# Optimization experiments

Hardware: AMD Instinct MI355X
Metric: run time of the kernel (lower is better)

## Reference

```python
import jax, jax.numpy as jnp
import numpy as np

NUM_CLASSES = 8
SCORE_T = 0.5
IOU_T = 0.5
POSE_HYPS = 10
MAX_DET = 100
B, A = 1, 4096


def _pairwise_iou(bx):
    # bx: (N,4) in (x1,y1,x2,y2); TF-style +1 pixel convention
    x1 = jnp.maximum(bx[:, None, 0], bx[None, :, 0])
    y1 = jnp.maximum(bx[:, None, 1], bx[None, :, 1])
    x2 = jnp.minimum(bx[:, None, 2], bx[None, :, 2])
    y2 = jnp.minimum(bx[:, None, 3], bx[None, :, 3])
    wid = x2 - x1 + 1.0
    hei = y2 - y1 + 1.0
    inter = wid * hei
    area = (bx[:, 2] - bx[:, 0] + 1.0) * (bx[:, 3] - bx[:, 1] + 1.0)
    den = area[:, None] + area[None, :] - inter
    ov = jnp.where(den == 0.0, 0.0, inter / jnp.where(den == 0.0, 1.0, den))  # divide_no_nan
    return jnp.where((wid <= 0.0) | (hei <= 0.0), 0.0, ov)


def _per_class(scores_c, boxes_c, poses_c, conf_c):
    # Fixed-shape re-expression of _filter_detections: instead of compacting the
    # boxes with score > threshold (dynamic shape), keep all N and mask invalid
    # boxes out of the overlap indicator. Relative ordering (which drives the
    # argmax tie-break and the ascending sort) is identical to the compacted
    # subset, so the math matches exactly.
    N = scores_c.shape[0]
    K = POSE_HYPS + 1
    valid = scores_c > SCORE_T
    m = jnp.sum(valid.astype(jnp.int32))  # number of selected boxes
    ov = _pairwise_iou(boxes_c)  # (N,N)
    ind = ((ov > IOU_T) & valid[:, None] & valid[None, :]).astype(jnp.float32)
    # scatter_nd: true_ov[argmax_col(row i), i] = max(row i); column i is unique per update
    max_col = jnp.argmax(ind, axis=1)
    true_ov = jnp.zeros_like(ind).at[max_col, jnp.arange(N)].add(jnp.max(ind, axis=1))
    bc = (1.0 - ov) * true_ov * conf_c[None, :]
    bc = jnp.where(bc == 0.0, 1000.0, bc)  # 1000 = sentinel for 'not a hypothesis'
    # Only the first min(pose_hyps+1, m) ascending-sorted entries per row survive the
    # sequence mask, so take the K smallest instead of a full argsort (same result;
    # top_k of the negation breaks ties by lowest index like a stable ascending sort).
    neg, args = jax.lax.top_k(-bc, K)
    svals = -neg  # (N,K) K smallest per row
    hyp = (jnp.arange(K) < jnp.minimum(K, m)).astype(jnp.float32)
    cmask = jnp.where(svals == 1000.0, 0.0, 1.0) * hyp[None, :]
    denom = jnp.sum(cmask, axis=1)  # (N,)
    safe = jnp.where(denom == 0.0, 1.0, denom)
    poses_avg = jnp.where(denom[:, None] == 0.0, 0.0,
                          jnp.sum(cmask[:, :, None] * poses_c[args], axis=1) / safe[:, None])
    boxes_avg = jnp.where(denom[:, None] == 0.0, 0.0,
                          jnp.sum(cmask[:, :, None] * boxes_c[args], axis=1) / safe[:, None])
    return poses_avg, boxes_avg, denom > 0.0


def _forward(boxes3D, boxes, classification, poses, confidence):
    C = NUM_CLASSES
    N = classification.shape[0] * classification.shape[1]
    cls = classification.reshape(N, C)
    bxs = boxes.reshape(N, C, 4)
    pss = poses.reshape(N, C, 12)
    cnf = confidence.reshape(N, C)
    # boxes3D is reshaped/gathered by the original but never used afterwards (dead code)
    xs = (cls.T, jnp.transpose(bxs, (1, 0, 2)), jnp.transpose(pss, (1, 0, 2)), cnf.T)
    # serialize over classes so only one NxN working set is live at a time
    poses_avg, boxes_avg, survive = jax.lax.map(lambda t: _per_class(*t), xs)
    surv = survive.reshape(-1)  # (C*N,) class-major, matching the original concat order
    count = jnp.sum(surv.astype(jnp.int32))
    scores_flat = jnp.where(surv, cls.T.reshape(-1), -jnp.inf)
    top_scores, _ = jax.lax.top_k(scores_flat, MAX_DET)
    rank = jnp.arange(MAX_DET)
    ok = rank < count
    out_scores = jnp.where(ok, top_scores, -1.0)
    # NOTE: the original computes top_indices but never applies it — labels/poses/
    # indices/boxes stay in class-major survivor order, truncated/padded with -1.
    pos = jnp.arange(C * N)
    order = jnp.argsort(jnp.where(surv, pos, pos + C * N))  # stable compaction
    sel = order[:MAX_DET]
    labels_flat = jnp.repeat(jnp.arange(C), N)
    anchors_flat = jnp.tile(jnp.arange(N), C)
    out_labels = jnp.where(ok, labels_flat[sel], -1).astype(jnp.int32)
    out_idx = jnp.where(ok, anchors_flat[sel], -1).astype(jnp.int32)
    out_poses = jnp.where(ok[:, None], poses_avg.reshape(C * N, 12)[sel], -1.0)
    out_boxes = jnp.where(ok[:, None], boxes_avg.reshape(C * N, 4)[sel], -1.0)
    return out_scores, out_labels, out_poses, out_idx, out_boxes


def setup_inputs():
    key = jax.random.key(0)
    k1, k2, k3, k4, k5, k6 = jax.random.split(key, 6)
    C = NUM_CLASSES
    # realistic heavily-overlapping boxes in a 640x640 image
    cxy = jax.random.uniform(k1, (B, A, C, 2), minval=0.0, maxval=640.0)
    wh = jax.random.uniform(k2, (B, A, C, 2), minval=10.0, maxval=120.0)
    boxes = jnp.concatenate([cxy - wh / 2.0, cxy + wh / 2.0], axis=-1).reshape(B, A, C * 4)
    return {
        "boxes3D": jax.random.normal(k6, (B, A, C * 16), dtype=jnp.float32),
        "boxes": boxes,
        "classification": jax.random.uniform(k3, (B, A, C), dtype=jnp.float32),
        "poses": jax.random.normal(k4, (B, A, C * 12), dtype=jnp.float32),
        "confidence": jax.random.uniform(k5, (B, A, C), dtype=jnp.float32),
    }


def reference(boxes3D, boxes, classification, poses, confidence):
    return _forward(boxes3D, boxes, classification, poses, confidence)
```

## Files before the change

### kernel.cpp

```cpp
#include <hip/hip_runtime.h>
#include <stdint.h>

#define N_ANCH 4096
#define NCLS 8
#define CN (N_ANCH * NCLS)
#define SCORE_TH 0.5f
#define IOU_TH 0.5f
#define KSEL 11
#define MAX_DET 100
#define CAND_CAP 4096
#define TI 128
#define TJ 64
#define JOBS_PER_CLASS 1056

struct Params {
    const float* boxes; const float* cls; const float* poses; const float* conf;
    int* validList; int* mVal; int* minRank;
    int* surv; int* hist; int* blockCnt; int* gcnt;
    int* rep; int* sel; int* count_g; float* cand;
    float* out;
};

__device__ __forceinline__ float area_f(float4 b) {
    return (b.z - b.x + 1.0f) * (b.w - b.y + 1.0f);
}

__device__ __forceinline__ float iou_f(float4 a, float areaA, float4 b, float areaB) {
    float x1 = fmaxf(a.x, b.x);
    float y1 = fmaxf(a.y, b.y);
    float x2 = fminf(a.z, b.z);
    float y2 = fminf(a.w, b.w);
    float wid = x2 - x1 + 1.0f;
    float hei = y2 - y1 + 1.0f;
    float inter = wid * hei;
    float den = areaA + areaB - inter;
    float ov = (den == 0.0f) ? 0.0f : (inter / den);
    if (wid <= 0.0f || hei <= 0.0f) ov = 0.0f;
    return ov;
}

__global__ void __launch_bounds__(256) kS(Params p) {
    const int c = blockIdx.x;
    const int tid = threadIdx.x;
    const int lane = tid & 63, w = tid >> 6;
    const int cbase = c << 12;
    __shared__ unsigned long long smask[64];
    __shared__ int sbase[16];

    for (int ch = 0; ch < 16; ch++) {
        int n = ch * 256 + tid;
        int flag = (p.cls[n * 8 + c] > SCORE_TH) ? 1 : 0;
        unsigned long long m = __ballot(flag);
        if (lane == 0) smask[ch * 4 + w] = m;
    }
    __syncthreads();
    if (tid == 0) {
        int run = 0;
        for (int ch = 0; ch < 16; ch++) {
            sbase[ch] = run;
            run += __popcll(smask[ch * 4]) + __popcll(smask[ch * 4 + 1]) +
                   __popcll(smask[ch * 4 + 2]) + __popcll(smask[ch * 4 + 3]);
        }
        p.mVal[c] = run;
    }
    __syncthreads();
    for (int ch = 0; ch < 16; ch++) {
        unsigned long long m = smask[ch * 4 + w];
        if ((m >> lane) & 1ull) {
            int rank = __popcll(m & ((1ull << lane) - 1ull));
            int wb = 0;
            for (int i = 0; i < w; i++) wb += __popcll(smask[ch * 4 + i]);
            p.validList[c * N_ANCH + sbase[ch] + wb + rank] = ch * 256 + tid;
        }
    }
    for (int i = tid; i < N_ANCH; i += 256) {
        p.surv[cbase + i] = 0;
        p.minRank[cbase + i] = 0x7FFFFFFF;
    }
    if (c == 0) {
        for (int i = tid; i < 1024; i += 256) p.hist[i] = 0;
        if (tid < 128) p.blockCnt[tid] = 0;
        if (tid == 0) *p.gcnt = 0;
    }
}

__global__ void __launch_bounds__(128) kM(Params p) {
    int bid = blockIdx.x;
    int c = bid / JOBS_PER_CLASS;
    int t = bid - c * JOBS_PER_CLASS;
    int ci = (int)((sqrtf(4.0f * (float)t + 1.0f) - 1.0f) * 0.5f);
    while ((ci + 1) * (ci + 2) <= t) ci++;
    while (ci * (ci + 1) > t) ci--;
    int jt = t - ci * (ci + 1);
    int mc = p.mVal[c];
    int ib = ci * TI, jb = jt * TJ;
    if (ib >= mc || jb >= mc) return;
    int tid = threadIdx.x;
    int cbase = c << 12;
    const int* vl = p.validList + cbase;
    const float4* boxes4 = (const float4*)p.boxes;
    __shared__ float4 sB[TJ];
    __shared__ float sA[TJ];
    if (tid < TJ && jb + tid < mc) {
        int vj = vl[jb + tid];
        float4 b = boxes4[vj * 8 + c];
        sB[tid] = b;
        sA[tid] = area_f(b);
    }
    __syncthreads();
    int i = ib + tid;
    if (i >= mc) return;
    int limit = min(TJ, i - jb);
    limit = min(limit, mc - jb);
    if (limit <= 0) return;
    int k = vl[i];
    float4 bk = boxes4[k * 8 + c];
    float ak = area_f(bk);
    int lmin = 0x7FFFFFFF;
    #pragma unroll 4
    for (int r = 0; r < limit; r++) {
        float4 bj = sB[r];
        float x1 = fmaxf(bk.x, bj.x);
        float y1 = fmaxf(bk.y, bj.y);
        float x2 = fminf(bk.z, bj.z);
        float y2 = fminf(bk.w, bj.w);
        float wid = x2 - x1 + 1.0f;
        float hei = y2 - y1 + 1.0f;
        float inter = wid * hei;
        float den = ak + sA[r] - inter;
        bool m = (wid > 0.0f) && (hei > 0.0f) && (inter > 0.5f * den);
        if (m && r < lmin) lmin = r;
    }
    if (lmin != 0x7FFFFFFF) atomicMin(&p.minRank[cbase + i], jb + lmin);
}

__global__ void __launch_bounds__(256) kF(Params p) {
    int t = blockIdx.x * 256 + threadIdx.x;
    int c = t >> 12;
    int i = t & (N_ANCH - 1);
    if (i >= p.mVal[c]) return;
    int cbase = c << 12;
    const int* vl = p.validList + cbase;
    const float4* boxes4 = (const float4*)p.boxes;
    int k = vl[i];
    int mr = p.minRank[t];
    if (mr > i) mr = i;
    int ja = vl[mr];
    p.rep[cbase + k] = ja;
    if (mr < i) {
        float4 bk = boxes4[k * 8 + c];
        float4 bj = boxes4[ja * 8 + c];
        float ov = iou_f(bk, area_f(bk), bj, area_f(bj));
        float bcv = (1.0f - ov) * p.conf[k * 8 + c];
        if (bcv != 0.0f) {
            int old = atomicExch(&p.surv[cbase + ja], 1);
            if (old == 0) {
                atomicAdd(&p.blockCnt[(cbase + ja) >> 8], 1);
                unsigned bits = __float_as_uint(p.cls[ja * 8 + c]);
                int bb = (int)((bits - 0x3F000000u) >> 13);
                int bkt = bb < 0 ? 0 : (bb > 1023 ? 1023 : bb);
                atomicAdd(&p.hist[bkt], 1);
            }
        }
    }
}

__global__ void __launch_bounds__(256) kG(Params p) {
    const int bid = blockIdx.x;
    const int tid = threadIdx.x;
    const int lane = tid & 63, w = tid >> 6;
    __shared__ int sCnt[128];
    __shared__ int sSfx[256];
    __shared__ int s_misc[8];

    if (tid == 0) s_misc[0] = 0;
    if (tid < 128) sCnt[tid] = p.blockCnt[tid];
    int part = p.hist[4 * tid] + p.hist[4 * tid + 1] +
               p.hist[4 * tid + 2] + p.hist[4 * tid + 3];
    sSfx[tid] = part;
    __syncthreads();
    if (tid == 0) {
        int run = 0, myoff = 0;
        for (int i = 0; i < 128; i++) {
            if (i == bid) myoff = run;
            run += sCnt[i];
        }
        s_misc[1] = run;
        s_misc[2] = myoff;
        if (bid == 0) *p.count_g = run;
        int run2 = 0;
        for (int i = 255; i >= 0; i--) { int v = sSfx[i]; sSfx[i] = run2; run2 += v; }
    }
    __syncthreads();
    int count = s_misc[1];
    int target = count < MAX_DET ? count : MAX_DET;
    int S = sSfx[tid];
    int found = -1;
    for (int b = 4 * tid + 3; b >= 4 * tid; b--) {
        S += p.hist[b];
        if (found < 0 && S >= target) found = b;
    }
    if (found >= 0) atomicMax(&s_misc[0], found);
    __syncthreads();
    int t0 = s_misc[0];

    int q = bid * 256 + tid;
    int c = q >> 12, n = q & (N_ANCH - 1);
    int flag = p.surv[q] != 0;
    unsigned long long mask = __ballot(flag);
    if (lane == 0) s_misc[4 + w] = __popcll(mask);
    __syncthreads();
    int rank = __popcll(mask & ((1ull << lane) - 1ull));
    int wbase = 0;
    for (int i = 0; i < w; i++) wbase += s_misc[4 + i];
    int idx = s_misc[2] + wbase + rank;
    if (flag && idx < MAX_DET) p.sel[idx] = q;
    if (flag) {
        float sc = p.cls[n * 8 + c];
        unsigned bits = __float_as_uint(sc);
        int bb = (int)((bits - 0x3F000000u) >> 13);
        int bkt = bb < 0 ? 0 : (bb > 1023 ? 1023 : bb);
        if (bkt >= t0) {
            int id = atomicAdd(p.gcnt, 1);
            if (id < CAND_CAP) p.cand[id] = sc;
        }
    }
}

__global__ void __launch_bounds__(256) kO(Params p) {
    const int bid = blockIdx.x;
    const int tid = threadIdx.x;
    const int lane = tid & 63, w = tid >> 6;
    __shared__ __align__(16) unsigned char SMEM[32768];
    __shared__ int s_misc[8];
    __shared__ int s_ksel[KSEL];
    __shared__ unsigned long long s_red[5];
    const float4* boxes4 = (const float4*)p.boxes;

    if (bid == 0) {
        float* s = (float*)SMEM;
        int cc = *p.gcnt; if (cc > CAND_CAP) cc = CAND_CAP;
        int count = *p.count_g;
        int n = 128; while (n < cc) n <<= 1;
        for (int i = tid; i < n; i += 256) s[i] = (i < cc) ? -p.cand[i] : 1e38f;
        __syncthreads();
        for (int kk = 2; kk <= n; kk <<= 1) {
            for (int jj = kk >> 1; jj > 0; jj >>= 1) {
                for (int i = tid; i < n; i += 256) {
                    int ixj = i ^ jj;
                    if (ixj > i) {
                        float a = s[i], b2 = s[ixj];
                        bool up = ((i & kk) == 0);
                        if (up ? (a > b2) : (a < b2)) { s[i] = b2; s[ixj] = a; }
                    }
                }
                __syncthreads();
            }
        }
        if (tid < MAX_DET) p.out[tid] = (tid < count) ? -s[tid] : -1.0f;
    } else {
        int s = bid - 1;
        int count = *p.count_g;
        if (s >= count) {
            if (tid == 0) { p.out[100 + s] = -1.0f; p.out[1400 + s] = -1.0f; }
            if (tid < 12) p.out[200 + s * 12 + tid] = -1.0f;
            if (tid >= 16 && tid < 20) p.out[1500 + s * 4 + (tid - 16)] = -1.0f;
        } else {
            int sp = p.sel[s];
            int c = sp >> 12;
            int r = sp & (N_ANCH - 1);
            int cbase = c << 12;
            unsigned long long* keyArr = (unsigned long long*)SMEM;
            if (tid == 0) s_misc[0] = 0;
            __syncthreads();
            float4 br = boxes4[r * 8 + c];
            float ar = area_f(br);
            for (int k = tid; k < N_ANCH; k += 256) {
                if (k != r && p.cls[k * 8 + c] > SCORE_TH && p.rep[cbase + k] == r) {
                    float4 bkk = boxes4[k * 8 + c];
                    float ov = iou_f(br, ar, bkk, area_f(bkk));
                    float bcv = (1.0f - ov) * p.conf[k * 8 + c];
                    if (bcv != 0.0f) {
                        int id = atomicAdd(&s_misc[0], 1);
                        keyArr[id] = ((unsigned long long)__float_as_uint(bcv) << 32) | (unsigned)k;
                    }
                }
            }
            __syncthreads();
            int nm = s_misc[0];
            int dn = nm < KSEL ? nm : KSEL;
            unsigned long long lastBest = ~0ull;
            for (int j = 0; j < dn; j++) {
                unsigned long long bk = ~0ull;
                for (int i = tid; i < nm; i += 256) {
                    unsigned long long v = keyArr[i];
                    if (v == lastBest) { keyArr[i] = ~0ull; v = ~0ull; }
                    if (v < bk) bk = v;
                }
                for (int off = 32; off > 0; off >>= 1) {
                    unsigned long long o = __shfl_down(bk, off);
                    if (o < bk) bk = o;
                }
                if (lane == 0) s_red[w] = bk;
                __syncthreads();
                if (tid == 0) {
                    unsigned long long B = s_red[0];
                    for (int q2 = 1; q2 < 4; q2++) if (s_red[q2] < B) B = s_red[q2];
                    s_red[4] = B;
                    s_ksel[j] = (int)(B & 0xFFFFFFFFull);
                }
                __syncthreads();
                lastBest = s_red[4];
            }
            float fdn = (float)(dn > 0 ? dn : 1);
            if (tid < 12) {
                float ssum = 0.0f;
                for (int j = 0; j < dn; j++) {
                    int k = s_ksel[j];
                    ssum += p.poses[(k * 8 + c) * 12 + tid];
                }
                p.out[200 + s * 12 + tid] = ssum / fdn;
            } else if (tid < 16) {
                int d = tid - 12;
                float ssum = 0.0f;
                for (int j = 0; j < dn; j++) {
                    int k = s_ksel[j];
                    const float* bb2 = (const float*)&boxes4[k * 8 + c];
                    ssum += bb2[d];
                }
                p.out[1500 + s * 4 + d] = ssum / fdn;
            } else if (tid == 16) {
                p.out[100 + s] = (float)c;
            } else if (tid == 17) {
                p.out[1400 + s] = (float)r;
            }
        }
    }
}

extern "C" void kernel_launch(void* const* d_in, const int* in_sizes, int n_in,
                              void* d_out, int out_size, void* d_ws, size_t ws_size,
                              hipStream_t stream) {
    Params hp;
    hp.boxes = (const float*)d_in[1];
    hp.cls   = (const float*)d_in[2];
    hp.poses = (const float*)d_in[3];
    hp.conf  = (const float*)d_in[4];
    hp.out   = (float*)d_out;

    char* ws = (char*)d_ws;
    size_t off = 0;
    auto alloc = [&](size_t bytes) {
        void* pp = ws + off;
        off += (bytes + 255) & ~(size_t)255;
        return pp;
    };
    hp.validList = (int*)alloc(CN * sizeof(int));
    hp.mVal      = (int*)alloc(64);
    hp.minRank   = (int*)alloc(CN * sizeof(int));
    hp.surv      = (int*)alloc(CN * sizeof(int));
    hp.hist      = (int*)alloc(1024 * sizeof(int));
    hp.blockCnt  = (int*)alloc(128 * sizeof(int));
    hp.gcnt      = (int*)alloc(64);
    hp.rep       = (int*)alloc(CN * sizeof(int));
    hp.sel       = (int*)alloc(MAX_DET * sizeof(int));
    hp.count_g   = (int*)alloc(64);
    hp.cand      = (float*)alloc(CAND_CAP * sizeof(float));

    kS<<<NCLS, 256, 0, stream>>>(hp);
    kM<<<NCLS * JOBS_PER_CLASS, TI, 0, stream>>>(hp);
    kF<<<CN / 256, 256, 0, stream>>>(hp);
    kG<<<CN / 256, 256, 0, stream>>>(hp);
    kO<<<MAX_DET + 1, 256, 0, stream>>>(hp);
}
```

Baseline: 121.5 us.

## Fuse compaction/threshold kernel into output kernel, removing one launch

Removes the kG kernel and folds its work into kO. Every kO block recomputes the prefix sum of per-chunk survivor counts and then locates its own selected detection through a ballot over a single 256-entry chunk. Block 0 now does the histogram threshold and gathers candidates into shared memory by scanning all 32K survivor flags serially before the bitonic sort. This saves a kernel launch and its global scratch traffic, but block 0 takes on a 128-iteration scan that may lengthen the critical path.

```diff
diff --git a/kernel.cpp b/kernel.cpp
--- a/kernel.cpp
+++ b/kernel.cpp
@@ -16,8 +16,8 @@
 struct Params {
     const float* boxes; const float* cls; const float* poses; const float* conf;
     int* validList; int* mVal; int* minRank;
-    int* surv; int* hist; int* blockCnt; int* gcnt;
-    int* rep; int* sel; int* count_g; float* cand;
+    int* surv; int* hist; int* blockCnt;
+    int* rep;
     float* out;
 };
 
@@ -80,7 +80,6 @@
     if (c == 0) {
         for (int i = tid; i < 1024; i += 256) p.hist[i] = 0;
         if (tid < 128) p.blockCnt[tid] = 0;
-        if (tid == 0) *p.gcnt = 0;
     }
 }
 
@@ -165,84 +164,71 @@
     }
 }
 
-__global__ void __launch_bounds__(256) kG(Params p) {
-    const int bid = blockIdx.x;
-    const int tid = threadIdx.x;
-    const int lane = tid & 63, w = tid >> 6;
-    __shared__ int sCnt[128];
-    __shared__ int sSfx[256];
-    __shared__ int s_misc[8];
-
-    if (tid == 0) s_misc[0] = 0;
-    if (tid < 128) sCnt[tid] = p.blockCnt[tid];
-    int part = p.hist[4 * tid] + p.hist[4 * tid + 1] +
-               p.hist[4 * tid + 2] + p.hist[4 * tid + 3];
-    sSfx[tid] = part;
-    __syncthreads();
-    if (tid == 0) {
-        int run = 0, myoff = 0;
-        for (int i = 0; i < 128; i++) {
-            if (i == bid) myoff = run;
-            run += sCnt[i];
-        }
-        s_misc[1] = run;
-        s_misc[2] = myoff;
-        if (bid == 0) *p.count_g = run;
-        int run2 = 0;
-        for (int i = 255; i >= 0; i--) { int v = sSfx[i]; sSfx[i] = run2; run2 += v; }
-    }
-    __syncthreads();
-    int count = s_misc[1];
-    int target = count < MAX_DET ? count : MAX_DET;
-    int S = sSfx[tid];
-    int found = -1;
-    for (int b = 4 * tid + 3; b >= 4 * tid; b--) {
-        S += p.hist[b];
-        if (found < 0 && S >= target) found = b;
-    }
-    if (found >= 0) atomicMax(&s_misc[0], found);
-    __syncthreads();
-    int t0 = s_misc[0];
-
-    int q = bid * 256 + tid;
-    int c = q >> 12, n = q & (N_ANCH - 1);
-    int flag = p.surv[q] != 0;
-    unsigned long long mask = __ballot(flag);
-    if (lane == 0) s_misc[4 + w] = __popcll(mask);
-    __syncthreads();
-    int rank = __popcll(mask & ((1ull << lane) - 1ull));
-    int wbase = 0;
-    for (int i = 0; i < w; i++) wbase += s_misc[4 + i];
-    int idx = s_misc[2] + wbase + rank;
-    if (flag && idx < MAX_DET) p.sel[idx] = q;
-    if (flag) {
-        float sc = p.cls[n * 8 + c];
-        unsigned bits = __float_as_uint(sc);
-        int bb = (int)((bits - 0x3F000000u) >> 13);
-        int bkt = bb < 0 ? 0 : (bb > 1023 ? 1023 : bb);
-        if (bkt >= t0) {
-            int id = atomicAdd(p.gcnt, 1);
-            if (id < CAND_CAP) p.cand[id] = sc;
-        }
-    }
-}
-
 __global__ void __launch_bounds__(256) kO(Params p) {
     const int bid = blockIdx.x;
     const int tid = threadIdx.x;
     const int lane = tid & 63, w = tid >> 6;
     __shared__ __align__(16) unsigned char SMEM[32768];
+    __shared__ int sCnt[128];
+    __shared__ int sSfx[256];
     __shared__ int s_misc[8];
+    __shared__ int s_sp;
     __shared__ int s_ksel[KSEL];
     __shared__ unsigned long long s_red[5];
     const float4* boxes4 = (const float4*)p.boxes;
 
+    if (tid < 128) sCnt[tid] = p.blockCnt[tid];
+    __syncthreads();
+    if (tid == 0) {
+        int run = 0;
+        for (int i = 0; i < 128; i++) { int v = sCnt[i]; sCnt[i] = run; run += v; }
+        s_misc[1] = run;
+    }
+    __syncthreads();
+    int count = s_misc[1];
+
     if (bid == 0) {
+        if (tid == 0) s_misc[0] = 0;
+        int part = p.hist[4 * tid] + p.hist[4 * tid + 1] +
+                   p.hist[4 * tid + 2] + p.hist[4 * tid + 3];
+        sSfx[tid] = part;
+        __syncthreads();
+        if (tid == 0) {
+            int run2 = 0;
+            for (int i = 255; i >= 0; i--) { int v = sSfx[i]; sSfx[i] = run2; run2 += v; }
+        }
+        __syncthreads();
+        int target = count < MAX_DET ? count : MAX_DET;
+        int S = sSfx[tid];
+        int found = -1;
+        for (int b = 4 * tid + 3; b >= 4 * tid; b--) {
+            S += p.hist[b];
+            if (found < 0 && S >= target) found = b;
+        }
+        if (found >= 0) atomicMax(&s_misc[0], found);
+        __syncthreads();
+        int t0 = s_misc[0];
         float* s = (float*)SMEM;
-        int cc = *p.gcnt; if (cc > CAND_CAP) cc = CAND_CAP;
-        int count = *p.count_g;
+        if (tid == 0) s_misc[2] = 0;
+        __syncthreads();
+        for (int base = 0; base < CN; base += 256) {
+            int q = base + tid;
+            if (p.surv[q] != 0) {
+                int c = q >> 12, n = q & (N_ANCH - 1);
+                float sc = p.cls[n * 8 + c];
+                unsigned bits = __float_as_uint(sc);
+                int bb = (int)((bits - 0x3F000000u) >> 13);
+                int bkt = bb < 0 ? 0 : (bb > 1023 ? 1023 : bb);
+                if (bkt >= t0) {
+                    int id = atomicAdd(&s_misc[2], 1);
+                    if (id < CAND_CAP) s[id] = sc;
+                }
+            }
+        }
+        __syncthreads();
+        int cc = s_misc[2]; if (cc > CAND_CAP) cc = CAND_CAP;
         int n = 128; while (n < cc) n <<= 1;
-        for (int i = tid; i < n; i += 256) s[i] = (i < cc) ? -p.cand[i] : 1e38f;
+        for (int i = tid; i < n; i += 256) s[i] = (i < cc) ? -s[i] : 1e38f;
         __syncthreads();
         for (int kk = 2; kk <= n; kk <<= 1) {
             for (int jj = kk >> 1; jj > 0; jj >>= 1) {
@@ -259,14 +245,31 @@
         }
         if (tid < MAX_DET) p.out[tid] = (tid < count) ? -s[tid] : -1.0f;
     } else {
-        int s = bid - 1;
-        int count = *p.count_g;
-        if (s >= count) {
-            if (tid == 0) { p.out[100 + s] = -1.0f; p.out[1400 + s] = -1.0f; }
-            if (tid < 12) p.out[200 + s * 12 + tid] = -1.0f;
-            if (tid >= 16 && tid < 20) p.out[1500 + s * 4 + (tid - 16)] = -1.0f;
+        int sIdx = bid - 1;
+        if (sIdx >= count) {
+            if (tid == 0) { p.out[100 + sIdx] = -1.0f; p.out[1400 + sIdx] = -1.0f; }
+            if (tid < 12) p.out[200 + sIdx * 12 + tid] = -1.0f;
+            if (tid >= 16 && tid < 20) p.out[1500 + sIdx * 4 + (tid - 16)] = -1.0f;
         } else {
-            int sp = p.sel[s];
+            if (tid == 0) {
+                int ch = 0;
+                for (int i = 0; i < 128; i++) { if (sCnt[i] <= sIdx) ch = i; else break; }
+                s_misc[3] = ch;
+            }
+            __syncthreads();
+            int ch = s_misc[3];
+            int ls = sIdx - sCnt[ch];
+            int qq = ch * 256 + tid;
+            int flag = p.surv[qq] != 0;
+            unsigned long long m = __ballot(flag);
+            if (lane == 0) s_misc[4 + w] = __popcll(m);
+            __syncthreads();
+            int wbase = 0;
+            for (int i = 0; i < w; i++) wbase += s_misc[4 + i];
+            int rank = wbase + __popcll(m & ((1ull << lane) - 1ull));
+            if (flag && rank == ls) s_sp = qq;
+            __syncthreads();
+            int sp = s_sp;
             int c = sp >> 12;
             int r = sp & (N_ANCH - 1);
             int cbase = c << 12;
@@ -319,7 +322,7 @@
                     int k = s_ksel[j];
                     ssum += p.poses[(k * 8 + c) * 12 + tid];
                 }
-                p.out[200 + s * 12 + tid] = ssum / fdn;
+                p.out[200 + sIdx * 12 + tid] = ssum / fdn;
             } else if (tid < 16) {
                 int d = tid - 12;
                 float ssum = 0.0f;
@@ -328,11 +331,11 @@
                     const float* bb2 = (const float*)&boxes4[k * 8 + c];
                     ssum += bb2[d];
                 }
-                p.out[1500 + s * 4 + d] = ssum / fdn;
+                p.out[1500 + sIdx * 4 + d] = ssum / fdn;
             } else if (tid == 16) {
-                p.out[100 + s] = (float)c;
+                p.out[100 + sIdx] = (float)c;
             } else if (tid == 17) {
-                p.out[1400 + s] = (float)r;
+                p.out[1400 + sIdx] = (float)r;
             }
         }
     }
@@ -361,15 +364,10 @@
     hp.surv      = (int*)alloc(CN * sizeof(int));
     hp.hist      = (int*)alloc(1024 * sizeof(int));
     hp.blockCnt  = (int*)alloc(128 * sizeof(int));
-    hp.gcnt      = (int*)alloc(64);
     hp.rep       = (int*)alloc(CN * sizeof(int));
-    hp.sel       = (int*)alloc(MAX_DET * sizeof(int));
-    hp.count_g   = (int*)alloc(64);
-    hp.cand      = (float*)alloc(CAND_CAP * sizeof(float));
 
     kS<<<NCLS, 256, 0, stream>>>(hp);
     kM<<<NCLS * JOBS_PER_CLASS, TI, 0, stream>>>(hp);
     kF<<<CN / 256, 256, 0, stream>>>(hp);
-    kG<<<CN / 256, 256, 0, stream>>>(hp);
     kO<<<MAX_DET + 1, 256, 0, stream>>>(hp);
 }
```

Measured after the change: 163.6 us. 1.35x slower.
